# Optimization experiments

Hardware: AMD Instinct MI355X
Metric: run time of the kernel (lower is better)

## Reference

```python
import jax, jax.numpy as jnp
import numpy as np

# QConv2D (AngleMap feature map, entanglement-free PQC model):
# each 3x3 patch value x_q is angle-encoded as RY(w_q * x_q) on qubit q,
# then n_layers of trainable RZ(a)/RY(b) rotations are applied; the layer
# outputs the Bloch vector (<X>,<Y>,<Z>) of every qubit -> 3*n_qubits values
# per patch. Channel outputs are summed (Add), filters concatenated, relu.

KERNEL = (3, 3)
STRIDE = (1, 1)


def _extract_patches(x, k, s):
    # x: (B,H,W,C) -> (B,i0,i1,C,K) with K = k0*k1
    B, H, W, C = x.shape
    i0 = (H - k[0]) // s[0] + 1
    i1 = (W - k[1]) // s[1] + 1
    ri = jnp.arange(i0)[:, None] * s[0] + jnp.arange(k[0])[None, :]  # (i0,k0)
    rj = jnp.arange(i1)[:, None] * s[1] + jnp.arange(k[1])[None, :]  # (i1,k1)
    p = x[:, ri]            # (B,i0,k0,W,C)
    p = p[:, :, :, rj]      # (B,i0,k0,i1,k1,C)
    p = jnp.transpose(p, (0, 1, 3, 5, 2, 4))  # (B,i0,i1,C,k0,k1)
    return p.reshape(B, i0, i1, C, k[0] * k[1])


def setup_inputs() -> dict:
    key = jax.random.key(0)
    k_x, k_w, k_a, k_b = jax.random.split(key, 4)
    B, H, W, C = 32, 128, 128, 3
    F, Q, L = 2, KERNEL[0] * KERNEL[1], 2  # filters, n_qubits, n_layers
    input_tensor = jax.random.uniform(k_x, (B, H, W, C), dtype=jnp.float32)
    w_enc = jax.random.normal(k_w, (F, C, Q), dtype=jnp.float32)
    a_rz = jax.random.normal(k_a, (F, C, L, Q), dtype=jnp.float32)
    b_ry = jax.random.normal(k_b, (F, C, L, Q), dtype=jnp.float32)
    return {"input_tensor": input_tensor, "w_enc": w_enc, "a_rz": a_rz, "b_ry": b_ry}


def reference(input_tensor, w_enc, a_rz, b_ry):
    B = input_tensor.shape[0]
    F, C, Q = w_enc.shape
    L = a_rz.shape[2]
    patches = _extract_patches(input_tensor, KERNEL, STRIDE)  # (B,i0,i1,C,Q)
    i0, i1 = patches.shape[1], patches.shape[2]
    # angle encoding per (filter, channel, qubit)
    theta = patches[:, :, :, None, :, :] * w_enc[None, None, None]  # (B,i0,i1,F,C,Q)
    vx, vy, vz = jnp.sin(theta), jnp.zeros_like(theta), jnp.cos(theta)
    for l in range(L):  # small fixed layer count
        ca, sa = jnp.cos(a_rz[:, :, l]), jnp.sin(a_rz[:, :, l])  # (F,C,Q)
        cb, sb = jnp.cos(b_ry[:, :, l]), jnp.sin(b_ry[:, :, l])
        # RZ(a): rotate Bloch vector about Z
        vx, vy = vx * ca - vy * sa, vx * sa + vy * ca
        # RY(b): rotate about Y
        vx, vz = vx * cb + vz * sb, -vx * sb + vz * cb
    out = jnp.stack([vx, vy, vz], axis=-1)       # (B,i0,i1,F,C,Q,3)
    out = out.sum(axis=4)                        # Add over channels -> (B,i0,i1,F,Q,3)
    out = out.reshape(B, i0, i1, F * Q * 3)      # Concatenate over filters
    return jax.nn.relu(out)
```

## Files before the change

### kernel.cpp

```cpp
#include <hip/hip_runtime.h>
#include <math.h>

#define NB 32
#define NH 128
#define NW 128
#define NC 3
#define NF 2
#define NQ 9
#define NL 2
#define I0 126
#define I1 126
#define NPIX (NB * I0 * I1)
#define NWORK (NPIX * 18)
#define GTHREADS 1016064
#define DPIX 56448
#define INV2PI 0.15915494309189535f

struct f3 { float x, y, z; };

__global__ __launch_bounds__(256) void qconv_fused(
        const float* __restrict__ x,
        const float* __restrict__ w_enc,
        const float* __restrict__ a_rz,
        const float* __restrict__ b_ry,
        float* __restrict__ out) {
    __shared__ float stab[54 * 8];
    int tid = threadIdx.x;
    if (tid < 54) {
        int t = tid;
        int f = t / 27;
        int c = (t / 9) % 3;
        int q = t % 9;
        float ux = 1.f, uy = 0.f, uz = 0.f;
        float wx = 0.f, wy = 0.f, wz = 1.f;
#pragma unroll
        for (int l = 0; l < NL; ++l) {
            int ia = ((f * NC + c) * NL + l) * NQ + q;
            float sa, ca, sb, cb;
            __sincosf(a_rz[ia], &sa, &ca);
            __sincosf(b_ry[ia], &sb, &cb);
            float nx, ny, nz;
            nx = ux * ca - uy * sa; ny = ux * sa + uy * ca; ux = nx; uy = ny;
            nx = ux * cb + uz * sb; nz = -ux * sb + uz * cb; ux = nx; uz = nz;
            nx = wx * ca - wy * sa; ny = wx * sa + wy * ca; wx = nx; wy = ny;
            nx = wx * cb + wz * sb; nz = -wx * sb + wz * cb; wx = nx; wz = nz;
        }
        float* o = stab + t * 8;
        o[0] = w_enc[t] * INV2PI;
        o[1] = ux; o[2] = uy; o[3] = uz;
        o[4] = wx; o[5] = wy; o[6] = wz;
        o[7] = 0.f;
    }
    __syncthreads();

    int T0 = blockIdx.x * 256 + tid;
    int pixb = T0 / 18;
    int q18 = T0 - pixb * 18;
    int f = (q18 >= 9) ? 1 : 0;
    int q = q18 - f * 9;
    int di = q / 3, dj = q - di * 3;

    float cw[3], sx[3], sy[3], sz[3], cx[3], cy[3], cz[3];
#pragma unroll
    for (int c = 0; c < 3; ++c) {
        const float* r = stab + (size_t)(f * 27 + c * 9 + q) * 8;
        float4 v0 = *reinterpret_cast<const float4*>(r);
        float4 v1 = *reinterpret_cast<const float4*>(r + 4);
        cw[c] = v0.x; sx[c] = v0.y; sy[c] = v0.z; sz[c] = v0.w;
        cx[c] = v1.x; cy[c] = v1.y; cz[c] = v1.z;
    }

    int b   = pixb / (I0 * I1);
    int rem = pixb - b * (I0 * I1);
    int i   = rem / I1;
    int j   = rem - i * I1;

    int icur = i;
    const float* pin = x + ((size_t)((b * NH + i + di) * NW) + (j + dj)) * NC;
    float* pout = out + (size_t)pixb * 54 + q18 * 3;

    const long STEP_IN  = 454L * NW * NC;
    const long WRAP_IN  = 2L * NW * NC;
    const long STEP_OUT = (long)DPIX * 54;

#define ADVANCE()  do { icur += 70; pin += STEP_IN; \
                        if (icur >= I0) { icur -= I0; pin += WRAP_IN; } } while (0)

#define COMPUTE_STORE(P, OP) do {                                   \
        float a0 = 0.f, a1 = 0.f, a2 = 0.f;                         \
        _Pragma("unroll")                                           \
        for (int c = 0; c < 3; ++c) {                               \
            float pc = (c == 0) ? (P).x : (c == 1) ? (P).y : (P).z; \
            float xr = pc * cw[c];                                  \
            float s  = __builtin_amdgcn_sinf(xr);                   \
            float co = __builtin_amdgcn_cosf(xr);                   \
            a0 = fmaf(sx[c], s, fmaf(cx[c], co, a0));               \
            a1 = fmaf(sy[c], s, fmaf(cy[c], co, a1));               \
            a2 = fmaf(sz[c], s, fmaf(cz[c], co, a2));               \
        }                                                           \
        f3 r_;                                                      \
        r_.x = fmaxf(a0, 0.f);                                      \
        r_.y = fmaxf(a1, 0.f);                                      \
        r_.z = fmaxf(a2, 0.f);                                      \
        *reinterpret_cast<f3*>(OP) = r_;                            \
    } while (0)

#pragma unroll
    for (int g = 0; g < 3; ++g) {
        const float* pA = pin; ADVANCE();
        const float* pB = pin; ADVANCE();
        const float* pC = pin; ADVANCE();
        f3 PA = *reinterpret_cast<const f3*>(pA);
        f3 PB = *reinterpret_cast<const f3*>(pB);
        f3 PC = *reinterpret_cast<const f3*>(pC);

        COMPUTE_STORE(PA, pout);
        COMPUTE_STORE(PB, pout + STEP_OUT);
        COMPUTE_STORE(PC, pout + 2 * STEP_OUT);
        pout += 3 * STEP_OUT;
    }
#undef ADVANCE
#undef COMPUTE_STORE
}

extern "C" void kernel_launch(void* const* d_in, const int* in_sizes, int n_in,
                              void* d_out, int out_size, void* d_ws, size_t ws_size,
                              hipStream_t stream) {
    const float* x     = (const float*)d_in[0];
    const float* w_enc = (const float*)d_in[1];
    const float* a_rz  = (const float*)d_in[2];
    const float* b_ry  = (const float*)d_in[3];
    float* out = (float*)d_out;

    int block = 256;
    int grid = GTHREADS / block;
    qconv_fused<<<grid, block, 0, stream>>>(x, w_enc, a_rz, b_ry, out);
}
```

Before: 26.96 us.

## Assign nine horizontally adjacent pixels per thread instead of strided rows

Each thread now handles a group of 9 consecutive output pixels along a row, reading 27 contiguous input floats, instead of 9 pixels spread 70 rows apart. The goal is contiguous loads and stores per thread and simpler index arithmetic without the wrap logic. Within a warp, adjacent groups of 18 threads write 486-float blocks, so each store instruction's coalescing pattern changes. Register use grows by the 27-element buffer.

```diff
diff --git a/kernel.cpp b/kernel.cpp
--- a/kernel.cpp
+++ b/kernel.cpp
@@ -10,10 +10,9 @@
 #define NL 2
 #define I0 126
 #define I1 126
-#define NPIX (NB * I0 * I1)
-#define NWORK (NPIX * 18)
-#define GTHREADS 1016064
-#define DPIX 56448
+#define NGJ 14
+#define NGROUPS (NB * I0 * NGJ)
+#define GTHREADS (NGROUPS * 18)
 #define INV2PI 0.15915494309189535f
 
 struct f3 { float x, y, z; };
@@ -54,8 +53,8 @@
     __syncthreads();
 
     int T0 = blockIdx.x * 256 + tid;
-    int pixb = T0 / 18;
-    int q18 = T0 - pixb * 18;
+    int grp = T0 / 18;
+    int q18 = T0 - grp * 18;
     int f = (q18 >= 9) ? 1 : 0;
     int q = q18 - f * 9;
     int di = q / 3, dj = q - di * 3;
@@ -70,57 +69,39 @@
         cx[c] = v1.x; cy[c] = v1.y; cz[c] = v1.z;
     }
 
-    int b   = pixb / (I0 * I1);
-    int rem = pixb - b * (I0 * I1);
-    int i   = rem / I1;
-    int j   = rem - i * I1;
+    int b   = grp / (I0 * NGJ);
+    int rem = grp - b * (I0 * NGJ);
+    int i   = rem / NGJ;
+    int j   = (rem - i * NGJ) * 9;
 
-    int icur = i;
     const float* pin = x + ((size_t)((b * NH + i + di) * NW) + (j + dj)) * NC;
-    float* pout = out + (size_t)pixb * 54 + q18 * 3;
+    float* pout = out + (size_t)grp * 486 + q18 * 3;
 
-    const long STEP_IN  = 454L * NW * NC;
-    const long WRAP_IN  = 2L * NW * NC;
-    const long STEP_OUT = (long)DPIX * 54;
-
-#define ADVANCE()  do { icur += 70; pin += STEP_IN; \
-                        if (icur >= I0) { icur -= I0; pin += WRAP_IN; } } while (0)
-
-#define COMPUTE_STORE(P, OP) do {                                   \
-        float a0 = 0.f, a1 = 0.f, a2 = 0.f;                         \
-        _Pragma("unroll")                                           \
-        for (int c = 0; c < 3; ++c) {                               \
-            float pc = (c == 0) ? (P).x : (c == 1) ? (P).y : (P).z; \
-            float xr = pc * cw[c];                                  \
-            float s  = __builtin_amdgcn_sinf(xr);                   \
-            float co = __builtin_amdgcn_cosf(xr);                   \
-            a0 = fmaf(sx[c], s, fmaf(cx[c], co, a0));               \
-            a1 = fmaf(sy[c], s, fmaf(cy[c], co, a1));               \
-            a2 = fmaf(sz[c], s, fmaf(cz[c], co, a2));               \
-        }                                                           \
-        f3 r_;                                                      \
-        r_.x = fmaxf(a0, 0.f);                                      \
-        r_.y = fmaxf(a1, 0.f);                                      \
-        r_.z = fmaxf(a2, 0.f);                                      \
-        *reinterpret_cast<f3*>(OP) = r_;                            \
-    } while (0)
+    float p[27];
+#pragma unroll
+    for (int t = 0; t < 9; ++t) {
+        f3 v = *reinterpret_cast<const f3*>(pin + t * 3);
+        p[3 * t + 0] = v.x; p[3 * t + 1] = v.y; p[3 * t + 2] = v.z;
+    }
 
 #pragma unroll
-    for (int g = 0; g < 3; ++g) {
-        const float* pA = pin; ADVANCE();
-        const float* pB = pin; ADVANCE();
-        const float* pC = pin; ADVANCE();
-        f3 PA = *reinterpret_cast<const f3*>(pA);
-        f3 PB = *reinterpret_cast<const f3*>(pB);
-        f3 PC = *reinterpret_cast<const f3*>(pC);
-
-        COMPUTE_STORE(PA, pout);
-        COMPUTE_STORE(PB, pout + STEP_OUT);
-        COMPUTE_STORE(PC, pout + 2 * STEP_OUT);
-        pout += 3 * STEP_OUT;
+    for (int t = 0; t < 9; ++t) {
+        float a0 = 0.f, a1 = 0.f, a2 = 0.f;
+#pragma unroll
+        for (int c = 0; c < 3; ++c) {
+            float xr = p[3 * t + c] * cw[c];
+            float s  = __builtin_amdgcn_sinf(xr);
+            float co = __builtin_amdgcn_cosf(xr);
+            a0 = fmaf(sx[c], s, fmaf(cx[c], co, a0));
+            a1 = fmaf(sy[c], s, fmaf(cy[c], co, a1));
+            a2 = fmaf(sz[c], s, fmaf(cz[c], co, a2));
+        }
+        f3 r;
+        r.x = fmaxf(a0, 0.f);
+        r.y = fmaxf(a1, 0.f);
+        r.z = fmaxf(a2, 0.f);
+        *reinterpret_cast<f3*>(pout + t * 54) = r;
     }
-#undef ADVANCE
-#undef COMPUTE_STORE
 }
 
 extern "C" void kernel_launch(void* const* d_in, const int* in_sizes, int n_in,
```

Result: no change. 27.02 us (+0.2%).
